# Performance work log

Hardware: AMD Instinct MI355X
Metric: run time of the kernel (lower is better)

The kernel has to match this reference:

```python
import jax, jax.numpy as jnp
import numpy as np

B, S, D, H, FF = 2, 2048, 1024, 16, 4096
DH = D // H  # head dim


def _layernorm(x, g, b, eps=1e-5):
    m = x.mean(-1, keepdims=True)
    v = ((x - m) ** 2).mean(-1, keepdims=True)
    return (x - m) / jnp.sqrt(v + eps) * g + b


def setup_inputs() -> dict:
    key = jax.random.key(0)
    ks = jax.random.split(key, 10)
    s = 0.02
    return {
        "x": jax.random.normal(ks[0], (B, S, D), jnp.float32),
        "y": jax.random.normal(ks[1], (B, S, D), jnp.float32),
        "z": jax.random.normal(ks[2], (B, S, D), jnp.float32),
        "mask": jnp.ones((B, 1, S, S), jnp.int32),
        "Wq": jax.random.normal(ks[3], (D, D), jnp.float32) * s,
        "bq": jnp.zeros((D,), jnp.float32),
        "Wk": jax.random.normal(ks[4], (D, D), jnp.float32) * s,
        "bk": jnp.zeros((D,), jnp.float32),
        "Wv": jax.random.normal(ks[5], (D, D), jnp.float32) * s,
        "bv": jnp.zeros((D,), jnp.float32),
        "Wo": jax.random.normal(ks[6], (D, D), jnp.float32) * s,
        "bo": jnp.zeros((D,), jnp.float32),
        "W1": jax.random.normal(ks[7], (D, FF), jnp.float32) * s,
        "b1": jnp.zeros((FF,), jnp.float32),
        "W2": jax.random.normal(ks[8], (FF, D), jnp.float32) * s,
        "b2": jnp.zeros((D,), jnp.float32),
        "ln_g": jnp.ones((D,), jnp.float32),
        "ln_b": jnp.zeros((D,), jnp.float32),
    }


def reference(x, y, z, mask, Wq, bq, Wk, bk, Wv, bv, Wo, bo, W1, b1, W2, b2, ln_g, ln_b):
    q = (x @ Wq + bq).reshape(B, S, H, DH)
    k = (y @ Wk + bk).reshape(B, S, H, DH)
    v = (z @ Wv + bv).reshape(B, S, H, DH)
    # scores: [B, H, Q, K]
    scores = jnp.einsum('bqhl,bkhl->bhqk', q, k) / (DH ** 0.5)
    scores = jnp.where(mask == 0, jnp.float32(-1e10), scores)
    # NOTE: source softmaxes over dim=2 (the query axis) -- faithful.
    p = jax.nn.softmax(scores, axis=2)
    # Source einsum 'bhqk,bvhl->bvhl' sums p over q,k -> per-(b,h) scalar scaling v.
    s_bh = p.sum(axis=(2, 3))  # [B, H]
    att = s_bh[:, None, :, None] * v  # [B, S, H, DH]
    att = att.reshape(B, S, D) @ Wo + bo
    # shared AddAndNorm (same LayerNorm params used twice); dropout = identity (eval)
    h1 = _layernorm(z + att, ln_g, ln_b)
    ff = jax.nn.relu(h1 @ W1 + b1) @ W2 + b2
    return _layernorm(h1 + ff, ln_g, ln_b)
```

## Files before the change

kernel.cpp:

```cpp
#include <hip/hip_runtime.h>

static constexpr int kB = 2, kS = 2048, kD = 1024, kFF = 4096;
static constexpr int kM = kB * kS;
static constexpr size_t MB = 1u << 20;

typedef __attribute__((ext_vector_type(8))) short short8;
typedef __attribute__((ext_vector_type(4))) float f32x4;

__device__ __forceinline__ unsigned short f2bf(float f) {
  union { float f; unsigned int u; } c; c.f = f;
  unsigned int u = c.u;
  unsigned int r = u + 0x7FFFu + ((u >> 16) & 1u);
  return (unsigned short)(r >> 16);
}

__device__ __forceinline__ float bf2f(unsigned short b) {
  union { unsigned int u; float f; } c;
  c.u = ((unsigned int)b) << 16;
  return c.f;
}

__device__ __forceinline__ void gload_lds16(const void* g, void* l) {
  __builtin_amdgcn_global_load_lds(
      (const __attribute__((address_space(1))) void*)g,
      (__attribute__((address_space(3))) void*)l, 16, 0, 0);
}

__global__ __launch_bounds__(256) void cast_bf16_kernel(
    const float* __restrict__ in, unsigned short* __restrict__ out, int n) {
  int i = (blockIdx.x * 256 + threadIdx.x) * 4;
  if (i >= n) return;
  float4 v = *(const float4*)(in + i);
  ushort4 o;
  o.x = f2bf(v.x); o.y = f2bf(v.y); o.z = f2bf(v.z); o.w = f2bf(v.w);
  *(ushort4*)(out + i) = o;
}

__global__ __launch_bounds__(256) void cast_transpose64(
    const float* __restrict__ W, unsigned short* __restrict__ Wt,
    int K, int N, float scale, int ntN) {
  __shared__ float tile[64][65];
  const int bid = blockIdx.x;
  const int nb = (bid % ntN) * 64, kb = (bid / ntN) * 64;
  const int tx = threadIdx.x & 15, ty = threadIdx.x >> 4;
#pragma unroll
  for (int p = 0; p < 4; ++p) {
    const int r = ty + 16 * p;
    float4 v = *(const float4*)(W + (size_t)(kb + r) * N + nb + tx * 4);
    tile[r][tx * 4 + 0] = v.x;
    tile[r][tx * 4 + 1] = v.y;
    tile[r][tx * 4 + 2] = v.z;
    tile[r][tx * 4 + 3] = v.w;
  }
  __syncthreads();
#pragma unroll
  for (int p = 0; p < 4; ++p) {
    const int n = ty + 16 * p;
    ushort4 o;
    o.x = f2bf(tile[tx * 4 + 0][n] * scale);
    o.y = f2bf(tile[tx * 4 + 1][n] * scale);
    o.z = f2bf(tile[tx * 4 + 2][n] * scale);
    o.w = f2bf(tile[tx * 4 + 3][n] * scale);
    *(ushort4*)(Wt + (size_t)(nb + n) * K + kb + tx * 4) = o;
  }
}

__global__ __launch_bounds__(256) void bias_gemv_part_kernel(
    const float* __restrict__ bv, const float* __restrict__ Wo,
    float* __restrict__ partial) {
  const int b = blockIdx.x, t = threadIdx.x;
  const int c = t * 4;
  float4 acc = {0.f, 0.f, 0.f, 0.f};
#pragma unroll
  for (int r = 0; r < 8; ++r) {
    const int f = b * 8 + r;
    const float s = bv[f];
    float4 w = *(const float4*)(Wo + (size_t)f * 1024 + c);
    acc.x = fmaf(s, w.x, acc.x);
    acc.y = fmaf(s, w.y, acc.y);
    acc.z = fmaf(s, w.z, acc.z);
    acc.w = fmaf(s, w.w, acc.w);
  }
  *(float4*)(partial + (size_t)b * 1024 + c) = acc;
}

__global__ __launch_bounds__(256) void bias_gemv_fin_kernel(
    const float* __restrict__ partial, const float* __restrict__ bo,
    float* __restrict__ bc) {
  const int n = blockIdx.x * 256 + threadIdx.x;
  float acc = 0.0f;
#pragma unroll 8
  for (int b = 0; b < 128; ++b) acc += partial[(size_t)b * 1024 + n];
  bc[n] = 2048.0f * acc + bo[n];
}

__global__ __launch_bounds__(256) void combine_wc4_kernel(
    const unsigned short* __restrict__ P, unsigned short* __restrict__ Wt) {
  const int i = (blockIdx.x * 256 + threadIdx.x) * 4;
  const int MN = 1024 * 1024;
  ushort4 s0 = *(const ushort4*)(P + i);
  ushort4 s1 = *(const ushort4*)(P + MN + i);
  ushort4 s2 = *(const ushort4*)(P + 2 * MN + i);
  ushort4 s3 = *(const ushort4*)(P + 3 * MN + i);
  const int row = i >> 10, col = i & 1023;
  float v0 = bf2f(s0.x) + bf2f(s1.x) + bf2f(s2.x) + bf2f(s3.x) + (row == col + 0 ? 1.0f : 0.0f);
  float v1 = bf2f(s0.y) + bf2f(s1.y) + bf2f(s2.y) + bf2f(s3.y) + (row == col + 1 ? 1.0f : 0.0f);
  float v2 = bf2f(s0.z) + bf2f(s1.z) + bf2f(s2.z) + bf2f(s3.z) + (row == col + 2 ? 1.0f : 0.0f);
  float v3 = bf2f(s0.w) + bf2f(s1.w) + bf2f(s2.w) + bf2f(s3.w) + (row == col + 3 ? 1.0f : 0.0f);
  ushort4 o; o.x = f2bf(v0); o.y = f2bf(v1); o.z = f2bf(v2); o.w = f2bf(v3);
  *(ushort4*)(Wt + i) = o;
}

template <int OUT_BF16, int RELU, int A_F32>
__global__ __launch_bounds__(256, 4) void gemm_bt(
    const void* __restrict__ A, const unsigned short* __restrict__ Bt,
    const float* __restrict__ bias, void* __restrict__ Cout,
    int M, int N, int K, int nXtiles, int nTilesPerSplit, int kSplitLen,
    size_t cStride, int cr, int cc) {
  __shared__ __align__(16) unsigned short sA[128 * 64];
  __shared__ __align__(16) unsigned short sB[128 * 64];
  const unsigned short* Ab = (const unsigned short*)A;
  const float* Af = (const float*)A;
  const int tid = threadIdx.x;
  const int wave = tid >> 6, lane = tid & 63;
  const int wr = wave >> 1, wc = wave & 1;

  const int x = blockIdx.x & 7, j = blockIdx.x >> 3;
  const int bpc = cr * cc;
  const int chunkIdx = x + 8 * (j / bpc);
  const int w = j % bpc;
  const int chunksPerSplit = nTilesPerSplit / bpc;
  const int split = chunkIdx / chunksPerSplit;
  const int cL = chunkIdx % chunksPerSplit;
  const int cpr = nXtiles / cc;
  const int m0 = ((cL / cpr) * cr + w / cc) * 128;
  const int n0 = ((cL % cpr) * cc + w % cc) * 128;
  const int kBeg = split * kSplitLen, kEnd = kBeg + kSplitLen;

  const int srow = lane >> 3;
  const int scol = ((lane & 7) ^ srow) * 8;

  f32x4 acc[4][4] = {};

  for (int k0 = kBeg; k0 < kEnd; k0 += 64) {
    if constexpr (A_F32) {
      float4 pa[4][2];
#pragma unroll
      for (int i = 0; i < 4; ++i) {
        const int chunk = i * 4 + wave;
        const int rr = chunk * 8 + srow;
        const float* az = Af + (size_t)(m0 + rr) * K + (k0 + scol);
        pa[i][0] = *(const float4*)az;
        pa[i][1] = *(const float4*)(az + 4);
      }
#pragma unroll
      for (int i = 0; i < 4; ++i) {
        const int chunk = i * 4 + wave;
        short8 cv;
        cv[0] = (short)f2bf(pa[i][0].x); cv[1] = (short)f2bf(pa[i][0].y);
        cv[2] = (short)f2bf(pa[i][0].z); cv[3] = (short)f2bf(pa[i][0].w);
        cv[4] = (short)f2bf(pa[i][1].x); cv[5] = (short)f2bf(pa[i][1].y);
        cv[6] = (short)f2bf(pa[i][1].z); cv[7] = (short)f2bf(pa[i][1].w);
        *(short8*)&sA[chunk * 512 + lane * 8] = cv;
      }
    } else {
#pragma unroll
      for (int i = 0; i < 4; ++i) {
        const int chunk = i * 4 + wave;
        const int rr = chunk * 8 + srow;
        gload_lds16(Ab + (size_t)(m0 + rr) * K + (k0 + scol), &sA[chunk * 512]);
      }
    }
#pragma unroll
    for (int i = 0; i < 4; ++i) {
      const int chunk = i * 4 + wave;
      const int rr = chunk * 8 + srow;
      gload_lds16(Bt + (size_t)(n0 + rr) * K + (k0 + scol), &sB[chunk * 512]);
    }
    __syncthreads();
#pragma unroll
    for (int kk = 0; kk < 64; kk += 32) {
      const int kcol = kk + (lane >> 4) * 8;
      const int kswz = (lane & 7) * 8;
      short8 af[4], bfr[4];
#pragma unroll
      for (int m = 0; m < 4; ++m)
        af[m] = *(const short8*)&sA[(wr * 64 + m * 16 + (lane & 15)) * 64 + (kcol ^ kswz)];
#pragma unroll
      for (int n = 0; n < 4; ++n)
        bfr[n] = *(const short8*)&sB[(wc * 64 + n * 16 + (lane & 15)) * 64 + (kcol ^ kswz)];
#pragma unroll
      for (int m = 0; m < 4; ++m)
#pragma unroll
        for (int n = 0; n < 4; ++n)
          acc[m][n] = __builtin_amdgcn_mfma_f32_16x16x32_bf16(af[m], bfr[n], acc[m][n], 0, 0, 0);
    }
    __syncthreads();
  }

  const int cl = lane & 15, rg = lane >> 4;
  const float* bptr = (split == 0) ? bias : nullptr;
#pragma unroll
  for (int n = 0; n < 4; ++n) {
    const int col = n0 + wc * 64 + n * 16 + cl;
    const float bias_v = bptr ? bptr[col] : 0.0f;
#pragma unroll
    for (int m = 0; m < 4; ++m) {
      const int rbase = m0 + wr * 64 + m * 16 + rg * 4;
#pragma unroll
      for (int j2 = 0; j2 < 4; ++j2) {
        float v = acc[m][n][j2] + bias_v;
        if (RELU) v = fmaxf(v, 0.0f);
        const size_t idx = split * cStride + (size_t)(rbase + j2) * N + col;
        if (OUT_BF16)
          ((unsigned short*)Cout)[idx] = f2bf(v);
        else
          ((float*)Cout)[idx] = v;
      }
    }
  }
}

__global__ __launch_bounds__(256) void ln4_bf16_kernel(
    const unsigned short* __restrict__ P, size_t pStr,
    const float* __restrict__ gg, const float* __restrict__ bb,
    unsigned short* __restrict__ Hb) {
  const int row = blockIdx.x, t = threadIdx.x;
  const size_t base = (size_t)row * 1024 + t * 4;
  ushort4 v0 = *(const ushort4*)(P + base);
  ushort4 v1 = *(const ushort4*)(P + pStr + base);
  ushort4 v2 = *(const ushort4*)(P + 2 * pStr + base);
  ushort4 v3 = *(const ushort4*)(P + 3 * pStr + base);
  float a0 = bf2f(v0.x) + bf2f(v1.x) + bf2f(v2.x) + bf2f(v3.x);
  float a1 = bf2f(v0.y) + bf2f(v1.y) + bf2f(v2.y) + bf2f(v3.y);
  float a2 = bf2f(v0.z) + bf2f(v1.z) + bf2f(v2.z) + bf2f(v3.z);
  float a3 = bf2f(v0.w) + bf2f(v1.w) + bf2f(v2.w) + bf2f(v3.w);
  float s = a0 + a1 + a2 + a3;
  float ss = a0 * a0 + a1 * a1 + a2 * a2 + a3 * a3;
#pragma unroll
  for (int off = 32; off > 0; off >>= 1) {
    s += __shfl_down(s, off);
    ss += __shfl_down(ss, off);
  }
  __shared__ float rs[4], rss[4];
  __shared__ float smean, srstd;
  const int wave = t >> 6, lane = t & 63;
  if (lane == 0) { rs[wave] = s; rss[wave] = ss; }
  __syncthreads();
  if (t == 0) {
    float S1 = rs[0] + rs[1] + rs[2] + rs[3];
    float S2 = rss[0] + rss[1] + rss[2] + rss[3];
    float mean = S1 * (1.0f / 1024.0f);
    float var = S2 * (1.0f / 1024.0f) - mean * mean;
    smean = mean;
    srstd = rsqrtf(var + 1e-5f);
  }
  __syncthreads();
  const float mean = smean, rstd = srstd;
  float4 gv = *(const float4*)(gg + t * 4);
  float4 bv = *(const float4*)(bb + t * 4);
  ushort4 hb;
  hb.x = f2bf((a0 - mean) * rstd * gv.x + bv.x);
  hb.y = f2bf((a1 - mean) * rstd * gv.y + bv.y);
  hb.z = f2bf((a2 - mean) * rstd * gv.z + bv.z);
  hb.w = f2bf((a3 - mean) * rstd * gv.w + bv.w);
  *(ushort4*)(Hb + base) = hb;
}

__global__ __launch_bounds__(256) void ln_fin4_kernel(
    const unsigned short* __restrict__ Res, const unsigned short* __restrict__ P,
    size_t pStr, const float* __restrict__ gg, const float* __restrict__ bb,
    float* __restrict__ out) {
  const int row = blockIdx.x, t = threadIdx.x;
  const size_t base = (size_t)row * 1024 + t * 4;
  ushort4 rv = *(const ushort4*)(Res + base);
  ushort4 v0 = *(const ushort4*)(P + base);
  ushort4 v1 = *(const ushort4*)(P + pStr + base);
  ushort4 v2 = *(const ushort4*)(P + 2 * pStr + base);
  ushort4 v3 = *(const ushort4*)(P + 3 * pStr + base);
  float a0 = bf2f(rv.x) + bf2f(v0.x) + bf2f(v1.x) + bf2f(v2.x) + bf2f(v3.x);
  float a1 = bf2f(rv.y) + bf2f(v0.y) + bf2f(v1.y) + bf2f(v2.y) + bf2f(v3.y);
  float a2 = bf2f(rv.z) + bf2f(v0.z) + bf2f(v1.z) + bf2f(v2.z) + bf2f(v3.z);
  float a3 = bf2f(rv.w) + bf2f(v0.w) + bf2f(v1.w) + bf2f(v2.w) + bf2f(v3.w);
  float s = a0 + a1 + a2 + a3;
  float ss = a0 * a0 + a1 * a1 + a2 * a2 + a3 * a3;
#pragma unroll
  for (int off = 32; off > 0; off >>= 1) {
    s += __shfl_down(s, off);
    ss += __shfl_down(ss, off);
  }
  __shared__ float rs[4], rss[4];
  __shared__ float smean, srstd;
  const int wave = t >> 6, lane = t & 63;
  if (lane == 0) { rs[wave] = s; rss[wave] = ss; }
  __syncthreads();
  if (t == 0) {
    float S1 = rs[0] + rs[1] + rs[2] + rs[3];
    float S2 = rss[0] + rss[1] + rss[2] + rss[3];
    float mean = S1 * (1.0f / 1024.0f);
    float var = S2 * (1.0f / 1024.0f) - mean * mean;
    smean = mean;
    srstd = rsqrtf(var + 1e-5f);
  }
  __syncthreads();
  const float mean = smean, rstd = srstd;
  float4 gv = *(const float4*)(gg + t * 4);
  float4 bv = *(const float4*)(bb + t * 4);
  float4 ov;
  ov.x = (a0 - mean) * rstd * gv.x + bv.x;
  ov.y = (a1 - mean) * rstd * gv.y + bv.y;
  ov.z = (a2 - mean) * rstd * gv.z + bv.z;
  ov.w = (a3 - mean) * rstd * gv.w + bv.w;
  *(float4*)(out + base) = ov;
}

extern "C" void kernel_launch(void* const* d_in, const int* in_sizes, int n_in,
                              void* d_out, int out_size, void* d_ws, size_t ws_size,
                              hipStream_t stream) {
  const float* z  = (const float*)d_in[2];
  const float* Wv = (const float*)d_in[8];
  const float* bv = (const float*)d_in[9];
  const float* Wo = (const float*)d_in[10];
  const float* bo = (const float*)d_in[11];
  const float* W1 = (const float*)d_in[12];
  const float* b1 = (const float*)d_in[13];
  const float* W2 = (const float*)d_in[14];
  const float* b2 = (const float*)d_in[15];
  const float* lng = (const float*)d_in[16];
  const float* lnb = (const float*)d_in[17];
  float* out = (float*)d_out;

  char* ws = (char*)d_ws;
  unsigned short* a1   = (unsigned short*)(ws + 0 * MB);
  unsigned short* attP = (unsigned short*)(ws + 32 * MB);
  unsigned short* ffP  = (unsigned short*)(ws + 32 * MB);
  unsigned short* wcpB = (unsigned short*)(ws + 64 * MB);
  unsigned short* W2T  = (unsigned short*)(ws + 64 * MB);
  unsigned short* WoT  = (unsigned short*)(ws + 88 * MB);
  unsigned short* WvBf = (unsigned short*)(ws + 90 * MB);
  unsigned short* WcT  = (unsigned short*)(ws + 92 * MB);
  float*          bc   = (float*)(ws + 94 * MB);
  float*          bprt = (float*)(ws + 94 * MB + 65536);
  unsigned short* h1bf = (unsigned short*)(ws + 96 * MB);
  unsigned short* W1T  = (unsigned short*)(ws + 104 * MB);

  const size_t pStr = (size_t)kM * kD;
  const size_t wStr = (size_t)kD * kD;

  cast_transpose64<<<dim3(256), dim3(256), 0, stream>>>(
      Wo, WoT, kD, kD, (float)kS, kD / 64);
  cast_bf16_kernel<<<dim3(kD * kD / 1024), dim3(256), 0, stream>>>(Wv, WvBf, kD * kD);
  bias_gemv_part_kernel<<<dim3(128), dim3(256), 0, stream>>>(bv, Wo, bprt);
  bias_gemv_fin_kernel<<<dim3(4), dim3(256), 0, stream>>>(bprt, bo, bc);

  gemm_bt<1, 0, 0><<<dim3(256), dim3(256), 0, stream>>>(
      WoT, WvBf, nullptr, wcpB, kD, kD, kD, kD / 128, 64, 256, wStr, 8, 4);
  combine_wc4_kernel<<<dim3(1024), dim3(256), 0, stream>>>(wcpB, WcT);

  gemm_bt<1, 0, 1><<<dim3(1024), dim3(256), 0, stream>>>(
      z, WcT, bc, attP, kM, kD, kD, kD / 128, 256, 256, pStr, 8, 8);

  ln4_bf16_kernel<<<dim3(kM), dim3(256), 0, stream>>>(attP, pStr, lng, lnb, h1bf);

  cast_transpose64<<<dim3(1024), dim3(256), 0, stream>>>(
      W1, W1T, kD, kFF, 1.0f, kFF / 64);
  gemm_bt<1, 1, 0><<<dim3(1024), dim3(256), 0, stream>>>(
      h1bf, W1T, b1, a1, kM, kFF, kD, kFF / 128, 1024, kD, 0, 16, 8);

  cast_transpose64<<<dim3(1024), dim3(256), 0, stream>>>(
      W2, W2T, kFF, kD, 1.0f, kD / 64);
  gemm_bt<1, 0, 0><<<dim3(1024), dim3(256), 0, stream>>>(
      a1, W2T, b2, ffP, kM, kD, kFF, kD / 128, 256, kFF / 4, pStr, 16, 8);

  ln_fin4_kernel<<<dim3(kM), dim3(256), 0, stream>>>(h1bf, ffP, pStr, lng, lnb, out);
}
```

Before: 159.8 us.

## Merge weight-prep kernels into one launch and use per-wave LayerNorm rows

```diff
diff --git a/kernel.cpp b/kernel.cpp
--- a/kernel.cpp
+++ b/kernel.cpp
@@ -5,6 +5,7 @@
 static constexpr size_t MB = 1u << 20;
 
 typedef __attribute__((ext_vector_type(8))) short short8;
+typedef __attribute__((ext_vector_type(8))) unsigned short ushort8;
 typedef __attribute__((ext_vector_type(4))) float f32x4;
 
 __device__ __forceinline__ unsigned short f2bf(float f) {
@@ -26,22 +27,10 @@
       (__attribute__((address_space(3))) void*)l, 16, 0, 0);
 }
 
-__global__ __launch_bounds__(256) void cast_bf16_kernel(
-    const float* __restrict__ in, unsigned short* __restrict__ out, int n) {
-  int i = (blockIdx.x * 256 + threadIdx.x) * 4;
-  if (i >= n) return;
-  float4 v = *(const float4*)(in + i);
-  ushort4 o;
-  o.x = f2bf(v.x); o.y = f2bf(v.y); o.z = f2bf(v.z); o.w = f2bf(v.w);
-  *(ushort4*)(out + i) = o;
-}
-
-__global__ __launch_bounds__(256) void cast_transpose64(
+__device__ __forceinline__ void do_ct64(
     const float* __restrict__ W, unsigned short* __restrict__ Wt,
-    int K, int N, float scale, int ntN) {
-  __shared__ float tile[64][65];
-  const int bid = blockIdx.x;
-  const int nb = (bid % ntN) * 64, kb = (bid / ntN) * 64;
+    int K, int N, float scale, int ntN, int b, float (*tile)[65]) {
+  const int nb = (b % ntN) * 64, kb = (b / ntN) * 64;
   const int tx = threadIdx.x & 15, ty = threadIdx.x >> 4;
 #pragma unroll
   for (int p = 0; p < 4; ++p) {
@@ -65,37 +54,49 @@
   }
 }
 
-__global__ __launch_bounds__(256) void bias_gemv_part_kernel(
-    const float* __restrict__ bv, const float* __restrict__ Wo,
-    float* __restrict__ partial) {
-  const int b = blockIdx.x, t = threadIdx.x;
-  const int c = t * 4;
-  float4 acc = {0.f, 0.f, 0.f, 0.f};
-#pragma unroll
-  for (int r = 0; r < 8; ++r) {
-    const int f = b * 8 + r;
-    const float s = bv[f];
-    float4 w = *(const float4*)(Wo + (size_t)f * 1024 + c);
-    acc.x = fmaf(s, w.x, acc.x);
-    acc.y = fmaf(s, w.y, acc.y);
-    acc.z = fmaf(s, w.z, acc.z);
-    acc.w = fmaf(s, w.w, acc.w);
-  }
-  *(float4*)(partial + (size_t)b * 1024 + c) = acc;
-}
-
-__global__ __launch_bounds__(256) void bias_gemv_fin_kernel(
-    const float* __restrict__ partial, const float* __restrict__ bo,
+__global__ __launch_bounds__(256) void prep_kernel(
+    const float* __restrict__ Wo, const float* __restrict__ Wv,
+    const float* __restrict__ W1, const float* __restrict__ W2,
+    const float* __restrict__ bv,
+    unsigned short* __restrict__ WoT, unsigned short* __restrict__ WvBf,
+    unsigned short* __restrict__ W1T, unsigned short* __restrict__ W2T,
+    float* __restrict__ bprt) {
+  __shared__ float tile[64][65];
+  const int b = blockIdx.x;
+  if (b < 256) {
+    do_ct64(Wo, WoT, kD, kD, (float)kS, 16, b, tile);
+  } else if (b < 1280) {
+    do_ct64(W1, W1T, kD, kFF, 1.0f, 64, b - 256, tile);
+  } else if (b < 2304) {
+    do_ct64(W2, W2T, kFF, kD, 1.0f, 16, b - 1280, tile);
+  } else if (b < 3328) {
+    const int i = ((b - 2304) * 256 + threadIdx.x) * 4;
+    float4 v = *(const float4*)(Wv + i);
+    ushort4 o;
+    o.x = f2bf(v.x); o.y = f2bf(v.y); o.z = f2bf(v.z); o.w = f2bf(v.w);
+    *(ushort4*)(WvBf + i) = o;
+  } else {
+    const int bb = b - 3328, t = threadIdx.x;
+    const int c = t * 4;
+    float4 acc = {0.f, 0.f, 0.f, 0.f};
+#pragma unroll
+    for (int r = 0; r < 8; ++r) {
+      const int f = bb * 8 + r;
+      const float s = bv[f];
+      float4 w = *(const float4*)(Wo + (size_t)f * 1024 + c);
+      acc.x = fmaf(s, w.x, acc.x);
+      acc.y = fmaf(s, w.y, acc.y);
+      acc.z = fmaf(s, w.z, acc.z);
+      acc.w = fmaf(s, w.w, acc.w);
+    }
+    *(float4*)(bprt + (size_t)bb * 1024 + c) = acc;
+  }
+}
+
+__global__ __launch_bounds__(256) void combine_wc4_fin_kernel(
+    const unsigned short* __restrict__ P, unsigned short* __restrict__ Wt,
+    const float* __restrict__ bprt, const float* __restrict__ bo,
     float* __restrict__ bc) {
-  const int n = blockIdx.x * 256 + threadIdx.x;
-  float acc = 0.0f;
-#pragma unroll 8
-  for (int b = 0; b < 128; ++b) acc += partial[(size_t)b * 1024 + n];
-  bc[n] = 2048.0f * acc + bo[n];
-}
-
-__global__ __launch_bounds__(256) void combine_wc4_kernel(
-    const unsigned short* __restrict__ P, unsigned short* __restrict__ Wt) {
   const int i = (blockIdx.x * 256 + threadIdx.x) * 4;
   const int MN = 1024 * 1024;
   ushort4 s0 = *(const ushort4*)(P + i);
@@ -109,6 +110,13 @@
   float v3 = bf2f(s0.w) + bf2f(s1.w) + bf2f(s2.w) + bf2f(s3.w) + (row == col + 3 ? 1.0f : 0.0f);
   ushort4 o; o.x = f2bf(v0); o.y = f2bf(v1); o.z = f2bf(v2); o.w = f2bf(v3);
   *(ushort4*)(Wt + i) = o;
+  if (blockIdx.x < 4) {
+    const int n = blockIdx.x * 256 + threadIdx.x;
+    float acc = 0.0f;
+#pragma unroll 8
+    for (int bb = 0; bb < 128; ++bb) acc += bprt[(size_t)bb * 1024 + n];
+    bc[n] = 2048.0f * acc + bo[n];
+  }
 }
 
 template <int OUT_BF16, int RELU, int A_F32>
@@ -221,97 +229,107 @@
   }
 }
 
-__global__ __launch_bounds__(256) void ln4_bf16_kernel(
+__global__ __launch_bounds__(256) void ln4_wave_kernel(
     const unsigned short* __restrict__ P, size_t pStr,
     const float* __restrict__ gg, const float* __restrict__ bb,
     unsigned short* __restrict__ Hb) {
-  const int row = blockIdx.x, t = threadIdx.x;
-  const size_t base = (size_t)row * 1024 + t * 4;
-  ushort4 v0 = *(const ushort4*)(P + base);
-  ushort4 v1 = *(const ushort4*)(P + pStr + base);
-  ushort4 v2 = *(const ushort4*)(P + 2 * pStr + base);
-  ushort4 v3 = *(const ushort4*)(P + 3 * pStr + base);
-  float a0 = bf2f(v0.x) + bf2f(v1.x) + bf2f(v2.x) + bf2f(v3.x);
-  float a1 = bf2f(v0.y) + bf2f(v1.y) + bf2f(v2.y) + bf2f(v3.y);
-  float a2 = bf2f(v0.z) + bf2f(v1.z) + bf2f(v2.z) + bf2f(v3.z);
-  float a3 = bf2f(v0.w) + bf2f(v1.w) + bf2f(v2.w) + bf2f(v3.w);
-  float s = a0 + a1 + a2 + a3;
-  float ss = a0 * a0 + a1 * a1 + a2 * a2 + a3 * a3;
+  const int wave = threadIdx.x >> 6, lane = threadIdx.x & 63;
+  const int row = blockIdx.x * 4 + wave;
+  const size_t rbase = (size_t)row * 1024;
+  float a[16];
+#pragma unroll
+  for (int sw = 0; sw < 2; ++sw) {
+    const size_t idx = rbase + sw * 512 + lane * 8;
+    ushort8 v0 = *(const ushort8*)(P + idx);
+    ushort8 v1 = *(const ushort8*)(P + pStr + idx);
+    ushort8 v2 = *(const ushort8*)(P + 2 * pStr + idx);
+    ushort8 v3 = *(const ushort8*)(P + 3 * pStr + idx);
+#pragma unroll
+    for (int j = 0; j < 8; ++j)
+      a[sw * 8 + j] = bf2f(v0[j]) + bf2f(v1[j]) + bf2f(v2[j]) + bf2f(v3[j]);
+  }
+  float s = 0.f, ss = 0.f;
+#pragma unroll
+  for (int j = 0; j < 16; ++j) { s += a[j]; ss += a[j] * a[j]; }
 #pragma unroll
   for (int off = 32; off > 0; off >>= 1) {
     s += __shfl_down(s, off);
     ss += __shfl_down(ss, off);
   }
-  __shared__ float rs[4], rss[4];
-  __shared__ float smean, srstd;
-  const int wave = t >> 6, lane = t & 63;
-  if (lane == 0) { rs[wave] = s; rss[wave] = ss; }
-  __syncthreads();
-  if (t == 0) {
-    float S1 = rs[0] + rs[1] + rs[2] + rs[3];
-    float S2 = rss[0] + rss[1] + rss[2] + rss[3];
-    float mean = S1 * (1.0f / 1024.0f);
-    float var = S2 * (1.0f / 1024.0f) - mean * mean;
-    smean = mean;
-    srstd = rsqrtf(var + 1e-5f);
-  }
-  __syncthreads();
-  const float mean = smean, rstd = srstd;
-  float4 gv = *(const float4*)(gg + t * 4);
-  float4 bv = *(const float4*)(bb + t * 4);
-  ushort4 hb;
-  hb.x = f2bf((a0 - mean) * rstd * gv.x + bv.x);
-  hb.y = f2bf((a1 - mean) * rstd * gv.y + bv.y);
-  hb.z = f2bf((a2 - mean) * rstd * gv.z + bv.z);
-  hb.w = f2bf((a3 - mean) * rstd * gv.w + bv.w);
-  *(ushort4*)(Hb + base) = hb;
-}
-
-__global__ __launch_bounds__(256) void ln_fin4_kernel(
+  s = __shfl(s, 0);
+  ss = __shfl(ss, 0);
+  const float mean = s * (1.0f / 1024.0f);
+  const float rstd = rsqrtf(ss * (1.0f / 1024.0f) - mean * mean + 1e-5f);
+#pragma unroll
+  for (int sw = 0; sw < 2; ++sw) {
+    const int cbase = sw * 512 + lane * 8;
+    float4 g0 = *(const float4*)(gg + cbase);
+    float4 g1 = *(const float4*)(gg + cbase + 4);
+    float4 b0 = *(const float4*)(bb + cbase);
+    float4 b1 = *(const float4*)(bb + cbase + 4);
+    const float* gp0 = &g0.x; const float* gp1 = &g1.x;
+    const float* bp0 = &b0.x; const float* bp1 = &b1.x;
+    ushort8 o;
+#pragma unroll
+    for (int j = 0; j < 4; ++j) {
+      o[j]     = f2bf((a[sw * 8 + j]     - mean) * rstd * gp0[j] + bp0[j]);
+      o[4 + j] = f2bf((a[sw * 8 + 4 + j] - mean) * rstd * gp1[j] + bp1[j]);
+    }
+    *(ushort8*)(Hb + rbase + cbase) = o;
+  }
+}
+
+__global__ __launch_bounds__(256) void ln_fin_wave_kernel(
     const unsigned short* __restrict__ Res, const unsigned short* __restrict__ P,
     size_t pStr, const float* __restrict__ gg, const float* __restrict__ bb,
     float* __restrict__ out) {
-  const int row = blockIdx.x, t = threadIdx.x;
-  const size_t base = (size_t)row * 1024 + t * 4;
-  ushort4 rv = *(const ushort4*)(Res + base);
-  ushort4 v0 = *(const ushort4*)(P + base);
-  ushort4 v1 = *(const ushort4*)(P + pStr + base);
-  ushort4 v2 = *(const ushort4*)(P + 2 * pStr + base);
-  ushort4 v3 = *(const ushort4*)(P + 3 * pStr + base);
-  float a0 = bf2f(rv.x) + bf2f(v0.x) + bf2f(v1.x) + bf2f(v2.x) + bf2f(v3.x);
-  float a1 = bf2f(rv.y) + bf2f(v0.y) + bf2f(v1.y) + bf2f(v2.y) + bf2f(v3.y);
-  float a2 = bf2f(rv.z) + bf2f(v0.z) + bf2f(v1.z) + bf2f(v2.z) + bf2f(v3.z);
-  float a3 = bf2f(rv.w) + bf2f(v0.w) + bf2f(v1.w) + bf2f(v2.w) + bf2f(v3.w);
-  float s = a0 + a1 + a2 + a3;
-  float ss = a0 * a0 + a1 * a1 + a2 * a2 + a3 * a3;
+  const int wave = threadIdx.x >> 6, lane = threadIdx.x & 63;
+  const int row = blockIdx.x * 4 + wave;
+  const size_t rbase = (size_t)row * 1024;
+  float a[16];
+#pragma unroll
+  for (int sw = 0; sw < 2; ++sw) {
+    const size_t idx = rbase + sw * 512 + lane * 8;
+    ushort8 rv = *(const ushort8*)(Res + idx);
+    ushort8 v0 = *(const ushort8*)(P + idx);
+    ushort8 v1 = *(const ushort8*)(P + pStr + idx);
+    ushort8 v2 = *(const ushort8*)(P + 2 * pStr + idx);
+    ushort8 v3 = *(const ushort8*)(P + 3 * pStr + idx);
+#pragma unroll
+    for (int j = 0; j < 8; ++j)
+      a[sw * 8 + j] = bf2f(rv[j]) + bf2f(v0[j]) + bf2f(v1[j]) + bf2f(v2[j]) + bf2f(v3[j]);
+  }
+  float s = 0.f, ss = 0.f;
+#pragma unroll
+  for (int j = 0; j < 16; ++j) { s += a[j]; ss += a[j] * a[j]; }
 #pragma unroll
   for (int off = 32; off > 0; off >>= 1) {
     s += __shfl_down(s, off);
     ss += __shfl_down(ss, off);
   }
-  __shared__ float rs[4], rss[4];
-  __shared__ float smean, srstd;
-  const int wave = t >> 6, lane = t & 63;
-  if (lane == 0) { rs[wave] = s; rss[wave] = ss; }
-  __syncthreads();
-  if (t == 0) {
-    float S1 = rs[0] + rs[1] + rs[2] + rs[3];
-    float S2 = rss[0] + rss[1] + rss[2] + rss[3];
-    float mean = S1 * (1.0f / 1024.0f);
-    float var = S2 * (1.0f / 1024.0f) - mean * mean;
-    smean = mean;
-    srstd = rsqrtf(var + 1e-5f);
-  }
-  __syncthreads();
-  const float mean = smean, rstd = srstd;
-  float4 gv = *(const float4*)(gg + t * 4);
-  float4 bv = *(const float4*)(bb + t * 4);
-  float4 ov;
-  ov.x = (a0 - mean) * rstd * gv.x + bv.x;
-  ov.y = (a1 - mean) * rstd * gv.y + bv.y;
-  ov.z = (a2 - mean) * rstd * gv.z + bv.z;
-  ov.w = (a3 - mean) * rstd * gv.w + bv.w;
-  *(float4*)(out + base) = ov;
+  s = __shfl(s, 0);
+  ss = __shfl(ss, 0);
+  const float mean = s * (1.0f / 1024.0f);
+  const float rstd = rsqrtf(ss * (1.0f / 1024.0f) - mean * mean + 1e-5f);
+#pragma unroll
+  for (int sw = 0; sw < 2; ++sw) {
+    const int cbase = sw * 512 + lane * 8;
+    float4 g0 = *(const float4*)(gg + cbase);
+    float4 g1 = *(const float4*)(gg + cbase + 4);
+    float4 b0 = *(const float4*)(bb + cbase);
+    float4 b1 = *(const float4*)(bb + cbase + 4);
+    const float* gp0 = &g0.x; const float* gp1 = &g1.x;
+    const float* bp0 = &b0.x; const float* bp1 = &b1.x;
+    float4 o0, o1;
+    float* op0 = &o0.x; float* op1 = &o1.x;
+#pragma unroll
+    for (int j = 0; j < 4; ++j) {
+      op0[j] = (a[sw * 8 + j]     - mean) * rstd * gp0[j] + bp0[j];
+      op1[j] = (a[sw * 8 + 4 + j] - mean) * rstd * gp1[j] + bp1[j];
+    }
+    *(float4*)(out + rbase + cbase) = o0;
+    *(float4*)(out + rbase + cbase + 4) = o1;
+  }
 }
 
 extern "C" void kernel_launch(void* const* d_in, const int* in_sizes, int n_in,
@@ -334,8 +352,8 @@
   unsigned short* a1   = (unsigned short*)(ws + 0 * MB);
   unsigned short* attP = (unsigned short*)(ws + 32 * MB);
   unsigned short* ffP  = (unsigned short*)(ws + 32 * MB);
-  unsigned short* wcpB = (unsigned short*)(ws + 64 * MB);
   unsigned short* W2T  = (unsigned short*)(ws + 64 * MB);
+  unsigned short* wcpB = (unsigned short*)(ws + 72 * MB);
   unsigned short* WoT  = (unsigned short*)(ws + 88 * MB);
   unsigned short* WvBf = (unsigned short*)(ws + 90 * MB);
   unsigned short* WcT  = (unsigned short*)(ws + 92 * MB);
@@ -347,30 +365,27 @@
   const size_t pStr = (size_t)kM * kD;
   const size_t wStr = (size_t)kD * kD;
 
-  cast_transpose64<<<dim3(256), dim3(256), 0, stream>>>(
-      Wo, WoT, kD, kD, (float)kS, kD / 64);
-  cast_bf16_kernel<<<dim3(kD * kD / 1024), dim3(256), 0, stream>>>(Wv, WvBf, kD * kD);
-  bias_gemv_part_kernel<<<dim3(128), dim3(256), 0, stream>>>(bv, Wo, bprt);
-  bias_gemv_fin_kernel<<<dim3(4), dim3(256), 0, stream>>>(bprt, bo, bc);
+  prep_kernel<<<dim3(3456), dim3(256), 0, stream>>>(
+      Wo, Wv, W1, W2, bv, WoT, WvBf, W1T, W2T, bprt);
 
   gemm_bt<1, 0, 0><<<dim3(256), dim3(256), 0, stream>>>(
       WoT, WvBf, nullptr, wcpB, kD, kD, kD, kD / 128, 64, 256, wStr, 8, 4);
-  combine_wc4_kernel<<<dim3(1024), dim3(256), 0, stream>>>(wcpB, WcT);
+
+  combine_wc4_fin_kernel<<<dim3(1024), dim3(256), 0, stream>>>(
+      wcpB, WcT, bprt, bo, bc);
 
   gemm_bt<1, 0, 1><<<dim3(1024), dim3(256), 0, stream>>>(
       z, WcT, bc, attP, kM, kD, kD, kD / 128, 256, 256, pStr, 8, 8);
 
-  ln4_bf16_kernel<<<dim3(kM), dim3(256), 0, stream>>>(attP, pStr, lng, lnb, h1bf);
-
-  cast_transpose64<<<dim3(1024), dim3(256), 0, stream>>>(
-      W1, W1T, kD, kFF, 1.0f, kFF / 64);
+  ln4_wave_kernel<<<dim3(kM / 4), dim3(256), 0, stream>>>(
+      attP, pStr, lng, lnb, h1bf);
+
   gemm_bt<1, 1, 0><<<dim3(1024), dim3(256), 0, stream>>>(
       h1bf, W1T, b1, a1, kM, kFF, kD, kFF / 128, 1024, kD, 0, 16, 8);
 
-  cast_transpose64<<<dim3(1024), dim3(256), 0, stream>>>(
-      W2, W2T, kFF, kD, 1.0f, kD / 64);
   gemm_bt<1, 0, 0><<<dim3(1024), dim3(256), 0, stream>>>(
       a1, W2T, b2, ffP, kM, kD, kFF, kD / 128, 256, kFF / 4, pStr, 16, 8);
 
-  ln_fin4_kernel<<<dim3(kM), dim3(256), 0, stream>>>(h1bf, ffP, pStr, lng, lnb, out);
-}
+  ln_fin_wave_kernel<<<dim3(kM / 4), dim3(256), 0, stream>>>(
+      h1bf, ffP, pStr, lng, lnb, out);
+}
```

Result: faster. 145.6 us, median of 3 (-8.9%).
